# Performance work log

Measured on AMD Instinct MI355X. Metric: run time of the kernel, lower is better.

The kernel has to match this reference:

```python
import jax, jax.numpy as jnp
import numpy as np

B, T, C = 4, 2048, 1024
H = 16
D = C // H  # head_dim = 64
SCALE = D ** -0.5


def setup_inputs() -> dict:
    key = jax.random.key(0)
    k1, k2, k3 = jax.random.split(key, 3)
    x = jax.random.normal(k1, (B, T, C), dtype=jnp.float32)
    w_qkv = jax.random.normal(k2, (C, 3 * C), dtype=jnp.float32) * (C ** -0.5)
    w_proj = jax.random.normal(k3, (C, C), dtype=jnp.float32) * (C ** -0.5)
    return {"x": x, "w_qkv": w_qkv, "w_proj": w_proj}


def reference(x, w_qkv, w_proj):
    Bx, Tx, Cx = x.shape
    qkv = x @ w_qkv                        # [B, T, 3C]
    q, k, v = jnp.split(qkv, 3, axis=-1)   # each [B, T, C]
    # [B, T, H, D] -> [B, H, T, D]
    q = q.reshape(Bx, Tx, H, D).transpose(0, 2, 1, 3)
    k = k.reshape(Bx, Tx, H, D).transpose(0, 2, 1, 3)
    v = v.reshape(Bx, Tx, H, D).transpose(0, 2, 1, 3)
    att = jnp.einsum('bhqd,bhkd->bhqk', q, k) * SCALE  # [B, H, T, T]
    causal = jnp.tril(jnp.ones((Tx, Tx), dtype=bool))
    att = jnp.where(causal[None, None], att, -jnp.inf)
    att = jax.nn.softmax(att, axis=-1)
    # dropout p=0.0 (eval-mode reference): identity
    y = jnp.einsum('bhqk,bhkd->bhqd', att, v)          # [B, H, T, D]
    y = y.transpose(0, 2, 1, 3).reshape(Bx, Tx, Cx)    # [B, T, C]
    return y @ w_proj
```

## Files before the change

### kernel.cpp

```cpp
#include <hip/hip_runtime.h>
#include <hip/hip_bf16.h>

#define Bdim 4
#define Tdim 2048
#define Cdim 1024
#define Hdim 16
#define Ddim 64
#define SCALE_Q 0.18033688011112042f

using f32x4  = __attribute__((ext_vector_type(4))) float;
using short8 = __attribute__((ext_vector_type(8))) short;

union U8 { uint4 v; unsigned short s[8]; };

__device__ __forceinline__ unsigned short f2bf(float f) {
  union { float f; unsigned int i; } x; x.f = f;
  unsigned int lsb = (x.i >> 16) & 1u;
  unsigned int r = x.i + 0x7fffu + lsb;
  return (unsigned short)(r >> 16);
}

__device__ __forceinline__ unsigned int pk_bf16(float lo, float hi) {
  union { __hip_bfloat162 h; unsigned int u; } c;
  c.h = __float22bfloat162_rn(make_float2(lo, hi));
  return c.u;
}

__device__ __forceinline__ float fexp2(float x) {
#if __has_builtin(__builtin_amdgcn_exp2f)
  return __builtin_amdgcn_exp2f(x);
#else
  return exp2f(x);
#endif
}

__device__ __forceinline__ void glds16(const unsigned short* g, unsigned short* l) {
  __builtin_amdgcn_global_load_lds(
      (const __attribute__((address_space(1))) void*)g,
      (__attribute__((address_space(3))) void*)l,
      16, 0, 0);
}

__device__ __forceinline__ int detect_fmt(const unsigned int* xw) {
  int cnt = 0;
  for (int i = 0; i < 64; i++) {
    unsigned int e = (xw[i] >> 7) & 0xFFu;
    if (e >= 100u && e <= 140u) cnt++;
  }
  return (cnt >= 40) ? 1 : 0;
}

__global__ void detect_kernel(const unsigned int* __restrict__ x, int* __restrict__ flag) {
  if (threadIdx.x == 0) *flag = detect_fmt(x);
}

__global__ __launch_bounds__(256) void prep_kernel(
    const void* __restrict__ x, const void* __restrict__ wq, const void* __restrict__ wp,
    unsigned short* __restrict__ X16, unsigned short* __restrict__ WqT,
    unsigned short* __restrict__ WpT, int* __restrict__ flag)
{
  __shared__ __align__(16) unsigned short Ts[64][72];
  __shared__ int sfmt;
  if (threadIdx.x == 0) {
    const int f = detect_fmt((const unsigned int*)x);
    sfmt = f;
    if (blockIdx.x == 0) *flag = f;
  }
  __syncthreads();
  const int fmt = sfmt;
  const unsigned bid = blockIdx.x;
  const int tid = threadIdx.x;

  if (bid < 4096u) {
    const size_t i = (size_t)bid * 256 + tid;
    if (fmt == 1) {
      *(uint4*)(X16 + i * 8) = *(const uint4*)((const unsigned short*)x + i * 8);
    } else {
      const float* s = (const float*)x + i * 8;
      float4 a = *(const float4*)(s);
      float4 b = *(const float4*)(s + 4);
      U8 o;
      o.s[0]=f2bf(a.x); o.s[1]=f2bf(a.y); o.s[2]=f2bf(a.z); o.s[3]=f2bf(a.w);
      o.s[4]=f2bf(b.x); o.s[5]=f2bf(b.y); o.s[6]=f2bf(b.z); o.s[7]=f2bf(b.w);
      *(uint4*)(X16 + i * 8) = o.v;
    }
    return;
  }

  const void* W; unsigned short* WT; int N, K, n0, k0;
  if (bid < 4864u) {
    const int t = bid - 4096;
    W = wq; WT = WqT; N = 3072; K = 1024;
    n0 = (t % 48) * 64; k0 = (t / 48) * 64;
  } else {
    const int t = bid - 4864;
    W = wp; WT = WpT; N = 1024; K = 1024;
    n0 = (t & 15) * 64; k0 = (t >> 4) * 64;
  }
  const int r = tid >> 2, c0 = (tid & 3) * 16;

  if (fmt == 0) {
    const float* Wf = (const float*)W + (size_t)(k0 + r) * N + n0 + c0;
    #pragma unroll
    for (int j4 = 0; j4 < 4; j4++) {
      float4 v = *(const float4*)(Wf + j4 * 4);
      Ts[r][c0 + j4*4 + 0] = f2bf(v.x);
      Ts[r][c0 + j4*4 + 1] = f2bf(v.y);
      Ts[r][c0 + j4*4 + 2] = f2bf(v.z);
      Ts[r][c0 + j4*4 + 3] = f2bf(v.w);
    }
  } else {
    const unsigned short* Wh = (const unsigned short*)W + (size_t)(k0 + r) * N + n0 + c0;
    uint4 v0 = *(const uint4*)(Wh);
    uint4 v1 = *(const uint4*)(Wh + 8);
    *(uint4*)&Ts[r][c0] = v0;
    *(uint4*)&Ts[r][c0 + 8] = v1;
  }
  __syncthreads();

  U8 o0, o1;
  #pragma unroll
  for (int j = 0; j < 8; j++) { o0.s[j] = Ts[c0 + j][r]; o1.s[j] = Ts[c0 + 8 + j][r]; }
  unsigned short* dst = WT + (size_t)(n0 + r) * K + k0 + c0;
  *(uint4*)(dst)     = o0.v;
  *(uint4*)(dst + 8) = o1.v;
}

__global__ __launch_bounds__(256) void gemm128d_kernel(
    const unsigned short* __restrict__ A16,
    const unsigned short* __restrict__ BT16,
    void* __restrict__ Cout,
    unsigned short* __restrict__ Qb,
    unsigned short* __restrict__ Kb,
    unsigned short* __restrict__ Vb,
    const int* __restrict__ flag,
    int M, int N, int K, int mode, int vT)
{
  __shared__ __align__(16) unsigned short As[2][128 * 32];
  __shared__ __align__(16) unsigned short Bs[2][128 * 32];

  const int fmt = *flag;
  const int tid  = threadIdx.x;
  const int wave = tid >> 6;
  const int lane = tid & 63;
  const int col  = lane & 15;
  const int quad = lane >> 4;
  const int m0 = blockIdx.x * 128;
  const int n0 = blockIdx.y * 128;
  const int wm = (wave >> 1) * 64;
  const int wn = (wave & 1) * 64;

  const int r4 = lane >> 2;
  const int schunk = ((lane & 3) ^ ((lane >> 3) & 3)) * 8;
  const int rsw = (quad ^ ((col >> 1) & 3)) * 8;

  f32x4 acc[4][4];
  #pragma unroll
  for (int i = 0; i < 4; i++)
    #pragma unroll
    for (int j = 0; j < 4; j++) acc[i][j] = (f32x4){0.f, 0.f, 0.f, 0.f};

  const unsigned short* ApA = A16  + (size_t)(m0 + wave * 32 + r4) * K + schunk;
  const unsigned short* ApB = ApA + (size_t)16 * K;
  const unsigned short* BpA = BT16 + (size_t)(n0 + wave * 32 + r4) * K + schunk;
  const unsigned short* BpB = BpA + (size_t)16 * K;

#define STAGE(BUF, KS) do { \
    glds16(ApA + (KS) * 32, &As[BUF][wave * 32 * 32]);        \
    glds16(ApB + (KS) * 32, &As[BUF][(wave * 32 + 16) * 32]); \
    glds16(BpA + (KS) * 32, &Bs[BUF][wave * 32 * 32]);        \
    glds16(BpB + (KS) * 32, &Bs[BUF][(wave * 32 + 16) * 32]); \
  } while (0)

#define COMPUTE(BUF) do { \
    short8 afr[4], bfr[4]; \
    _Pragma("unroll") \
    for (int mi = 0; mi < 4; mi++) \
      afr[mi] = *(const short8*)&As[BUF][(wm + mi * 16 + col) * 32 + rsw]; \
    _Pragma("unroll") \
    for (int ni = 0; ni < 4; ni++) \
      bfr[ni] = *(const short8*)&Bs[BUF][(wn + ni * 16 + col) * 32 + rsw]; \
    _Pragma("unroll") \
    for (int mi = 0; mi < 4; mi++) \
      _Pragma("unroll") \
      for (int ni = 0; ni < 4; ni++) \
        acc[mi][ni] = __builtin_amdgcn_mfma_f32_16x16x32_bf16(afr[mi], bfr[ni], acc[mi][ni], 0, 0, 0); \
  } while (0)

  const int NK = K >> 5;
  STAGE(0, 0);
  for (int ks = 0; ks < NK - 1; ++ks) {
    STAGE((ks + 1) & 1, ks + 1);
    asm volatile("s_waitcnt vmcnt(4)" ::: "memory");
    __builtin_amdgcn_s_barrier();
    __builtin_amdgcn_sched_barrier(0);
    COMPUTE(ks & 1);
    __builtin_amdgcn_sched_barrier(0);
    __builtin_amdgcn_s_barrier();
  }
  asm volatile("s_waitcnt vmcnt(0)" ::: "memory");
  __builtin_amdgcn_s_barrier();
  __builtin_amdgcn_sched_barrier(0);
  COMPUTE((NK - 1) & 1);
#undef STAGE
#undef COMPUTE

  if (mode == 1) {
    const int bb = m0 >> 11;
    const int tBase = (m0 & 2047) + wm;
    #pragma unroll
    for (int ni = 0; ni < 4; ni++) {
      const int n = n0 + wn + ni * 16 + col;
      const int which = n >> 10;
      const int rem = n & 1023;
      const int h = rem >> 6;
      const int d = rem & 63;
      if (which == 2 && vT) {
        unsigned short* base = Vb + (size_t)(bb * Hdim + h) * Tdim * Ddim
                                  + (size_t)d * Tdim + tBase;
        #pragma unroll
        for (int mi = 0; mi < 4; mi++) {
          const int t0 = mi * 16 + quad * 4;
          *(uint2*)(base + t0) = make_uint2(pk_bf16(acc[mi][ni][0], acc[mi][ni][1]),
                                            pk_bf16(acc[mi][ni][2], acc[mi][ni][3]));
        }
      } else {
        unsigned short* dstBase = (which == 0) ? Qb : (which == 1 ? Kb : Vb);
        const float scale = (which == 0) ? SCALE_Q : 1.f;
        dstBase += (size_t)(bb * Hdim + h) * Tdim * Ddim + d;
        #pragma unroll
        for (int mi = 0; mi < 4; mi++)
          #pragma unroll
          for (int i = 0; i < 4; i++) {
            const int t = tBase + mi * 16 + quad * 4 + i;
            dstBase[(size_t)t * Ddim] = f2bf(acc[mi][ni][i] * scale);
          }
      }
    }
  } else {
    #pragma unroll
    for (int mi = 0; mi < 4; mi++)
      #pragma unroll
      for (int ni = 0; ni < 4; ni++)
        #pragma unroll
        for (int i = 0; i < 4; i++) {
          const int m = m0 + wm + mi * 16 + quad * 4 + i;
          const int n = n0 + wn + ni * 16 + col;
          const float v = acc[mi][ni][i];
          if (fmt == 0) ((float*)Cout)[(size_t)m * N + n] = v;
          else ((unsigned short*)Cout)[(size_t)m * N + n] = f2bf(v);
        }
  }
}

#define BM 64
#define BN 64
#define BK 32
#define LDK 40

__global__ __launch_bounds__(256) void gemm64_kernel(
    const void* __restrict__ A,
    const void* __restrict__ Bw,
    void* __restrict__ Cout,
    unsigned short* __restrict__ Qb,
    unsigned short* __restrict__ Kb,
    unsigned short* __restrict__ Vb,
    const int* __restrict__ flag,
    int M, int N, int K, int mode, int aFmt, int outFmt, int aOff, int mOff)
{
  __shared__ __align__(16) unsigned short As[BM * LDK];
  __shared__ __align__(16) unsigned short Bs[BN * LDK];

  const int fmt = *flag;
  const int af  = (aFmt  == 2) ? fmt : aFmt;
  const int of  = (outFmt == 2) ? fmt : outFmt;

  const int tid  = threadIdx.x;
  const int wave = tid >> 6;
  const int lane = tid & 63;
  const int m0 = blockIdx.x * BM;
  const int n0 = blockIdx.y * BN;

  const int ar = tid >> 2;
  const int ak = (tid & 3) * 8;
  const int bk = tid >> 3;
  const int bn = (tid & 7) * 8;

  const int lr = lane & 15;
  const int lq = lane >> 4;

  f32x4 acc[4] = {{0,0,0,0},{0,0,0,0},{0,0,0,0},{0,0,0,0}};

  for (int k0 = 0; k0 < K; k0 += BK) {
    U8 a8;
    if (af == 1) {
      a8.v = *(const uint4*)((const unsigned short*)A + (size_t)(aOff + m0 + ar) * K + (k0 + ak));
    } else {
      const float* Af = (const float*)A + (size_t)(aOff + m0 + ar) * K + (k0 + ak);
      float4 x0 = *(const float4*)(Af);
      float4 x1 = *(const float4*)(Af + 4);
      a8.s[0] = f2bf(x0.x); a8.s[1] = f2bf(x0.y); a8.s[2] = f2bf(x0.z); a8.s[3] = f2bf(x0.w);
      a8.s[4] = f2bf(x1.x); a8.s[5] = f2bf(x1.y); a8.s[6] = f2bf(x1.z); a8.s[7] = f2bf(x1.w);
    }
    *(uint4*)(&As[ar * LDK + ak]) = a8.v;

    U8 b8;
    if (fmt == 1) {
      b8.v = *(const uint4*)((const unsigned short*)Bw + (size_t)(k0 + bk) * N + (n0 + bn));
    } else {
      const float* Bf = (const float*)Bw + (size_t)(k0 + bk) * N + (n0 + bn);
      float4 x0 = *(const float4*)(Bf);
      float4 x1 = *(const float4*)(Bf + 4);
      b8.s[0] = f2bf(x0.x); b8.s[1] = f2bf(x0.y); b8.s[2] = f2bf(x0.z); b8.s[3] = f2bf(x0.w);
      b8.s[4] = f2bf(x1.x); b8.s[5] = f2bf(x1.y); b8.s[6] = f2bf(x1.z); b8.s[7] = f2bf(x1.w);
    }
    #pragma unroll
    for (int i = 0; i < 8; i++) Bs[(bn + i) * LDK + bk] = b8.s[i];
    __syncthreads();

    short8 afrag = *(const short8*)(&As[(wave * 16 + lr) * LDK + lq * 8]);
    #pragma unroll
    for (int c = 0; c < 4; c++) {
      short8 bfrag = *(const short8*)(&Bs[(c * 16 + lr) * LDK + lq * 8]);
      acc[c] = __builtin_amdgcn_mfma_f32_16x16x32_bf16(afrag, bfrag, acc[c], 0, 0, 0);
    }
    __syncthreads();
  }

  #pragma unroll
  for (int c = 0; c < 4; c++) {
    #pragma unroll
    for (int i = 0; i < 4; i++) {
      const int m = m0 + wave * 16 + lq * 4 + i;
      const int n = n0 + c * 16 + lr;
      const float v = acc[c][i];
      if (mode == 0) {
        if (of == 0) ((float*)Cout)[(size_t)(mOff + m) * N + n] = v;
        else ((unsigned short*)Cout)[(size_t)(mOff + m) * N + n] = f2bf(v);
      } else {
        const int which = n >> 10;
        const int rem = n & 1023;
        const int h = rem >> 6;
        const int d = rem & 63;
        const int b = m >> 11;
        const int t = m & 2047;
        const size_t idx = ((size_t)(b * Hdim + h) * Tdim + t) * Ddim + d;
        if      (which == 0) Qb[idx] = f2bf(v * SCALE_Q);
        else if (which == 1) Kb[idx] = f2bf(v);
        else                 Vb[idx] = f2bf(v);
      }
    }
  }
}

__global__ __launch_bounds__(256) void attn128_kernel(
    const unsigned short* __restrict__ Qb,
    const unsigned short* __restrict__ Kb,
    const unsigned short* __restrict__ Vb,
    const unsigned short* __restrict__ VbT,
    unsigned short* __restrict__ Y)
{
  __shared__ __align__(16) unsigned short Ks[64 * 72];
  __shared__ __align__(16) unsigned short Vt[64 * 72];
  __shared__ __align__(16) unsigned short Pw[4][32 * 72];

  const int tid  = threadIdx.x;
  const int wave = tid >> 6;
  const int lane = tid & 63;
  const int col  = lane & 15;
  const int quad = lane >> 4;

  const int pair = blockIdx.x & 7;
  const int bh   = blockIdx.x >> 3;
  const size_t headOff = (size_t)bh * Tdim * Ddim;

  const int sr = tid >> 2;
  const int sc = (tid & 3) * 16;

  const int b = bh >> 4;
  const int h = bh & 15;

  const short8 onesf = {16256, 16256, 16256, 16256, 16256, 16256, 16256, 16256};

  #pragma unroll
  for (int half = 0; half < 2; half++) {
    const int qt = half ? (15 - pair) : pair;
    const int qb = qt * 128;
    const int nkt = (qb >> 6) + 2;
    const int rMin = qb + wave * 32;
    const int rMax = rMin + 31;

    short8 qf[2][2];
    #pragma unroll
    for (int mi = 0; mi < 2; mi++) {
      const unsigned short* Qr = Qb + headOff + (size_t)(rMin + mi * 16 + col) * Ddim;
      qf[mi][0] = *(const short8*)(Qr + quad * 8);
      qf[mi][1] = *(const short8*)(Qr + 32 + quad * 8);
    }

    f32x4 o_acc[2][4];
    f32x4 l_acc[2];
    #pragma unroll
    for (int mi = 0; mi < 2; mi++) {
      l_acc[mi] = (f32x4){0.f, 0.f, 0.f, 0.f};
      #pragma unroll
      for (int n = 0; n < 4; n++) o_acc[mi][n] = (f32x4){0.f, 0.f, 0.f, 0.f};
    }

    uint4 kr0, kr1, vr0, vr1;
    {
      const unsigned short* Kr = Kb + headOff + (size_t)sr * Ddim + sc;
      kr0 = *(const uint4*)(Kr);
      kr1 = *(const uint4*)(Kr + 8);
      if (VbT) {
        const unsigned short* Vr = VbT + headOff + (size_t)sr * Tdim + sc;
        vr0 = *(const uint4*)(Vr);
        vr1 = *(const uint4*)(Vr + 8);
      } else {
        const unsigned short* Vr = Vb + headOff + (size_t)sr * Ddim + sc;
        vr0 = *(const uint4*)(Vr);
        vr1 = *(const uint4*)(Vr + 8);
      }
    }

    for (int kt = 0; kt < nkt; kt++) {
      __syncthreads();
      *(uint4*)&Ks[sr * 72 + sc]     = kr0;
      *(uint4*)&Ks[sr * 72 + sc + 8] = kr1;
      if (VbT) {
        *(uint4*)&Vt[sr * 72 + sc]     = vr0;
        *(uint4*)&Vt[sr * 72 + sc + 8] = vr1;
      } else {
        U8 v0, v1; v0.v = vr0; v1.v = vr1;
        #pragma unroll
        for (int j = 0; j < 8; j++) {
          Vt[(sc + j) * 72 + sr]     = v0.s[j];
          Vt[(sc + 8 + j) * 72 + sr] = v1.s[j];
        }
      }
      __syncthreads();

      if (kt + 1 < nkt) {
        const int kb = (kt + 1) * 64;
        const unsigned short* Kr = Kb + headOff + (size_t)(kb + sr) * Ddim + sc;
        kr0 = *(const uint4*)(Kr);
        kr1 = *(const uint4*)(Kr + 8);
        if (VbT) {
          const unsigned short* Vr = VbT + headOff + (size_t)sr * Tdim + kb + sc;
          vr0 = *(const uint4*)(Vr);
          vr1 = *(const uint4*)(Vr + 8);
        } else {
          const unsigned short* Vr = Vb + headOff + (size_t)(kb + sr) * Ddim + sc;
          vr0 = *(const uint4*)(Vr);
          vr1 = *(const uint4*)(Vr + 8);
        }
      }

      const int ktb = kt * 64;
      if (ktb <= rMax) {
        f32x4 s_acc[4][2];
        __builtin_amdgcn_s_setprio(1);
        #pragma unroll
        for (int c = 0; c < 4; c++) {
          const unsigned short* Kl = &Ks[(c * 16 + col) * 72];
          short8 kf0 = *(const short8*)(Kl + quad * 8);
          short8 kf1 = *(const short8*)(Kl + 32 + quad * 8);
          #pragma unroll
          for (int mi = 0; mi < 2; mi++) {
            f32x4 z = {0.f, 0.f, 0.f, 0.f};
            z = __builtin_amdgcn_mfma_f32_16x16x32_bf16(kf0, qf[mi][0], z, 0, 0, 0);
            s_acc[c][mi] = __builtin_amdgcn_mfma_f32_16x16x32_bf16(kf1, qf[mi][1], z, 0, 0, 0);
          }
        }
        __builtin_amdgcn_s_setprio(0);

        if (ktb + 63 > rMin) {
          #pragma unroll
          for (int c = 0; c < 4; c++)
            #pragma unroll
            for (int mi = 0; mi < 2; mi++)
              #pragma unroll
              for (int i = 0; i < 4; i++)
                if (ktb + c * 16 + quad * 4 + i > rMin + mi * 16 + col)
                  s_acc[c][mi][i] = -1e30f;
        }

        #pragma unroll
        for (int mi = 0; mi < 2; mi++)
          #pragma unroll
          for (int c = 0; c < 4; c++) {
            const float p0 = fexp2(fminf(s_acc[c][mi][0], 80.f));
            const float p1 = fexp2(fminf(s_acc[c][mi][1], 80.f));
            const float p2 = fexp2(fminf(s_acc[c][mi][2], 80.f));
            const float p3 = fexp2(fminf(s_acc[c][mi][3], 80.f));
            const unsigned int u0 = pk_bf16(p0, p1);
            const unsigned int u1 = pk_bf16(p2, p3);
            uint2* dst = (uint2*)&Pw[wave][(mi * 16 + col) * 72 + c * 16 + quad * 4];
            *dst = make_uint2(u0, u1);
          }

        short8 pf[2][2];
        __builtin_amdgcn_s_setprio(1);
        #pragma unroll
        for (int mi = 0; mi < 2; mi++) {
          pf[mi][0] = *(const short8*)(&Pw[wave][(mi * 16 + col) * 72 + quad * 8]);
          pf[mi][1] = *(const short8*)(&Pw[wave][(mi * 16 + col) * 72 + 32 + quad * 8]);
          l_acc[mi] = __builtin_amdgcn_mfma_f32_16x16x32_bf16(pf[mi][0], onesf, l_acc[mi], 0, 0, 0);
          l_acc[mi] = __builtin_amdgcn_mfma_f32_16x16x32_bf16(pf[mi][1], onesf, l_acc[mi], 0, 0, 0);
        }
        #pragma unroll
        for (int n = 0; n < 4; n++) {
          const unsigned short* Vl = &Vt[(n * 16 + col) * 72];
          short8 vf0 = *(const short8*)(Vl + quad * 8);
          short8 vf1 = *(const short8*)(Vl + 32 + quad * 8);
          #pragma unroll
          for (int mi = 0; mi < 2; mi++) {
            o_acc[mi][n] = __builtin_amdgcn_mfma_f32_16x16x32_bf16(pf[mi][0], vf0, o_acc[mi][n], 0, 0, 0);
            o_acc[mi][n] = __builtin_amdgcn_mfma_f32_16x16x32_bf16(pf[mi][1], vf1, o_acc[mi][n], 0, 0, 0);
          }
        }
        __builtin_amdgcn_s_setprio(0);
      }
    }

    #pragma unroll
    for (int mi = 0; mi < 2; mi++)
      #pragma unroll
      for (int i = 0; i < 4; i++) {
        const float inv = 1.f / l_acc[mi][i];
        const int qrow = rMin + mi * 16 + quad * 4 + i;
        unsigned short* dst = Y + (size_t)(b * Tdim + qrow) * Cdim + h * Ddim;
        #pragma unroll
        for (int n = 0; n < 4; n++)
          dst[n * 16 + col] = f2bf(o_acc[mi][n][i] * inv);
      }
  }
}

extern "C" void kernel_launch(void* const* d_in, const int* in_sizes, int n_in,
                              void* d_out, int out_size, void* d_ws, size_t ws_size,
                              hipStream_t stream) {
  const void* x      = d_in[0];
  const void* w_qkv  = d_in[1];
  const void* w_proj = d_in[2];

  int* flag = (int*)d_ws;
  unsigned short* wsb = (unsigned short*)((char*)d_ws + 1024);

  const size_t HS = (size_t)Bdim * Hdim * Tdim * Ddim;
  const size_t FULL  = 1024 + 2 * (4 * HS + (size_t)3072 * 1024 + (size_t)1024 * 1024);
  const size_t FULL2 = FULL + 2 * HS;
  const size_t MONO  = 1024 + 2 * (4 * HS);

  dim3 blk(256);

  if (ws_size >= FULL) {
    unsigned short* Qb  = wsb;
    unsigned short* Kb  = Qb + HS;
    unsigned short* Vb  = Kb + HS;
    unsigned short* XY  = Vb + HS;
    unsigned short* WqT = XY + HS;
    unsigned short* WpT = WqT + (size_t)3072 * 1024;
    unsigned short* VbT = WpT + (size_t)1024 * 1024;
    const int M = Bdim * Tdim;

    prep_kernel<<<dim3(5120), blk, 0, stream>>>(x, w_qkv, w_proj, XY, WqT, WpT, flag);

    if (ws_size >= FULL2) {
      gemm128d_kernel<<<dim3(M / 128, 3072 / 128), blk, 0, stream>>>(
          XY, WqT, nullptr, Qb, Kb, VbT, flag, M, 3072, Cdim, 1, 1);
      attn128_kernel<<<dim3(Bdim * Hdim * 8), blk, 0, stream>>>(Qb, Kb, nullptr, VbT, XY);
    } else {
      gemm128d_kernel<<<dim3(M / 128, 3072 / 128), blk, 0, stream>>>(
          XY, WqT, nullptr, Qb, Kb, Vb, flag, M, 3072, Cdim, 1, 0);
      attn128_kernel<<<dim3(Bdim * Hdim * 8), blk, 0, stream>>>(Qb, Kb, Vb, nullptr, XY);
    }

    gemm128d_kernel<<<dim3(M / 128, Cdim / 128), blk, 0, stream>>>(
        XY, WpT, d_out, nullptr, nullptr, nullptr, flag, M, Cdim, Cdim, 0, 0);
  } else if (ws_size >= MONO) {
    detect_kernel<<<1, 64, 0, stream>>>((const unsigned int*)x, flag);
    const size_t HSb = (size_t)Hdim * Tdim * Ddim;
    unsigned short* Qb2 = wsb;
    unsigned short* Kb2 = Qb2 + HSb;
    unsigned short* Vb2 = Kb2 + HSb;
    unsigned short* Y2  = Vb2 + HSb;
    for (int b = 0; b < Bdim; b++) {
      gemm64_kernel<<<dim3(Tdim / BM, 3072 / BN), blk, 0, stream>>>(
          x, w_qkv, nullptr, Qb2, Kb2, Vb2, flag,
          Tdim, 3072, Cdim, 1, 2, 2, b * Tdim, 0);
      attn128_kernel<<<dim3(Hdim * 8), blk, 0, stream>>>(Qb2, Kb2, Vb2, nullptr, Y2);
      gemm64_kernel<<<dim3(Tdim / BM, Cdim / BN), blk, 0, stream>>>(
          Y2, w_proj, d_out, nullptr, nullptr, nullptr, flag,
          Tdim, Cdim, Cdim, 0, 1, 2, 0, b * Tdim);
    }
  } else {
    detect_kernel<<<1, 64, 0, stream>>>((const unsigned int*)x, flag);
    const size_t HSb = (size_t)Hdim * Tdim * Ddim;
    unsigned short* Qb = wsb;
    unsigned short* Kb = Qb + HSb;
    unsigned short* Vb = Kb + HSb;
    unsigned short* Y2 = Vb + HSb;

    for (int b = 0; b < Bdim; b++) {
      gemm64_kernel<<<dim3(Tdim / BM, 3072 / BN), blk, 0, stream>>>(
          x, w_qkv, nullptr, Qb, Kb, Vb, flag,
          Tdim, 3072, Cdim, 1, 2, 2, b * Tdim, 0);

      attn128_kernel<<<dim3(Hdim * 8), blk, 0, stream>>>(Qb, Kb, Vb, nullptr, Y2);

      gemm64_kernel<<<dim3(Tdim / BM, Cdim / BN), blk, 0, stream>>>(
          Y2, w_proj, d_out, nullptr, nullptr, nullptr, flag,
          Tdim, Cdim, Cdim, 0, 1, 2, 0, b * Tdim);
    }
  }
}
```

Before: 249.3 us.

## Double-buffer attention K/V tiles with direct global-to-LDS loads and XOR swizzle

Adds a new attention kernel for the transposed-V path. It double-buffers K and V tiles in LDS, fills them with direct global-to-LDS copies (glds16), and overlaps the next tile's load with the current tile's MFMA work through vmcnt waits. Unpadded LDS rows use an XOR swizzle instead of padding to avoid bank conflicts, and setprio hints are dropped, including from the legacy kernel. The fallback paths keep the old register-staged kernel. LDS use rises from the extra buffer, and there is a barrier at both ends of each tile iteration.

```diff
diff --git a/kernel.cpp b/kernel.cpp
--- a/kernel.cpp
+++ b/kernel.cpp
@@ -356,6 +356,162 @@
 __global__ __launch_bounds__(256) void attn128_kernel(
     const unsigned short* __restrict__ Qb,
     const unsigned short* __restrict__ Kb,
+    const unsigned short* __restrict__ VbT,
+    unsigned short* __restrict__ Y)
+{
+  __shared__ __align__(16) unsigned short Ks[2][64 * 64];
+  __shared__ __align__(16) unsigned short Vt[2][64 * 64];
+  __shared__ __align__(16) unsigned short Pw[4][32 * 64];
+
+  const int tid  = threadIdx.x;
+  const int wave = tid >> 6;
+  const int lane = tid & 63;
+  const int col  = lane & 15;
+  const int quad = lane >> 4;
+  const int cx   = col & 7;
+  const int ch0  = (quad ^ cx) * 8;
+  const int ch1  = ch0 ^ 32;
+
+  const int srow = lane >> 3;
+  const int sx   = ((lane & 7) ^ (srow & 7)) * 8;
+
+  const int pair = blockIdx.x & 7;
+  const int bh   = blockIdx.x >> 3;
+  const size_t headOff = (size_t)bh * Tdim * Ddim;
+  const int b = bh >> 4;
+  const int h = bh & 15;
+
+  const short8 onesf = {16256, 16256, 16256, 16256, 16256, 16256, 16256, 16256};
+
+#define ASTAGE(BUF, KB) do { \
+    const unsigned short* Ksrc = Kb + headOff + (size_t)((KB) + wave * 16 + srow) * Ddim + sx; \
+    glds16(Ksrc,            &Ks[BUF][(wave * 16) * 64]);      \
+    glds16(Ksrc + 8 * Ddim, &Ks[BUF][(wave * 16 + 8) * 64]);  \
+    const unsigned short* Vsrc = VbT + headOff + (size_t)(wave * 16 + srow) * Tdim + (KB) + sx; \
+    glds16(Vsrc,            &Vt[BUF][(wave * 16) * 64]);      \
+    glds16(Vsrc + 8 * Tdim, &Vt[BUF][(wave * 16 + 8) * 64]);  \
+  } while (0)
+
+  #pragma unroll
+  for (int half = 0; half < 2; half++) {
+    const int qt = half ? (15 - pair) : pair;
+    const int qb = qt * 128;
+    const int nkt = (qb >> 6) + 2;
+    const int rMin = qb + wave * 32;
+    const int rMax = rMin + 31;
+
+    short8 qf[2][2];
+    #pragma unroll
+    for (int mi = 0; mi < 2; mi++) {
+      const unsigned short* Qr = Qb + headOff + (size_t)(rMin + mi * 16 + col) * Ddim;
+      qf[mi][0] = *(const short8*)(Qr + quad * 8);
+      qf[mi][1] = *(const short8*)(Qr + 32 + quad * 8);
+    }
+
+    f32x4 o_acc[2][4];
+    f32x4 l_acc[2];
+    #pragma unroll
+    for (int mi = 0; mi < 2; mi++) {
+      l_acc[mi] = (f32x4){0.f, 0.f, 0.f, 0.f};
+      #pragma unroll
+      for (int n = 0; n < 4; n++) o_acc[mi][n] = (f32x4){0.f, 0.f, 0.f, 0.f};
+    }
+
+    ASTAGE(0, 0);
+    for (int kt = 0; kt < nkt; kt++) {
+      const int cur = kt & 1;
+      if (kt + 1 < nkt) {
+        ASTAGE(cur ^ 1, (kt + 1) * 64);
+        asm volatile("s_waitcnt vmcnt(4)" ::: "memory");
+      } else {
+        asm volatile("s_waitcnt vmcnt(0)" ::: "memory");
+      }
+      __builtin_amdgcn_s_barrier();
+      __builtin_amdgcn_sched_barrier(0);
+
+      const int ktb = kt * 64;
+      if (ktb <= rMax) {
+        f32x4 s_acc[4][2];
+        #pragma unroll
+        for (int c = 0; c < 4; c++) {
+          const unsigned short* Kl = &Ks[cur][(c * 16 + col) * 64];
+          short8 kf0 = *(const short8*)(Kl + ch0);
+          short8 kf1 = *(const short8*)(Kl + ch1);
+          #pragma unroll
+          for (int mi = 0; mi < 2; mi++) {
+            f32x4 z = {0.f, 0.f, 0.f, 0.f};
+            z = __builtin_amdgcn_mfma_f32_16x16x32_bf16(kf0, qf[mi][0], z, 0, 0, 0);
+            s_acc[c][mi] = __builtin_amdgcn_mfma_f32_16x16x32_bf16(kf1, qf[mi][1], z, 0, 0, 0);
+          }
+        }
+
+        if (ktb + 63 > rMin) {
+          #pragma unroll
+          for (int c = 0; c < 4; c++)
+            #pragma unroll
+            for (int mi = 0; mi < 2; mi++)
+              #pragma unroll
+              for (int i = 0; i < 4; i++)
+                if (ktb + c * 16 + quad * 4 + i > rMin + mi * 16 + col)
+                  s_acc[c][mi][i] = -1e30f;
+        }
+
+        #pragma unroll
+        for (int mi = 0; mi < 2; mi++)
+          #pragma unroll
+          for (int c = 0; c < 4; c++) {
+            const float p0 = fexp2(fminf(s_acc[c][mi][0], 80.f));
+            const float p1 = fexp2(fminf(s_acc[c][mi][1], 80.f));
+            const float p2 = fexp2(fminf(s_acc[c][mi][2], 80.f));
+            const float p3 = fexp2(fminf(s_acc[c][mi][3], 80.f));
+            const unsigned int u0 = pk_bf16(p0, p1);
+            const unsigned int u1 = pk_bf16(p2, p3);
+            const int po = (((c * 2 + (quad >> 1)) ^ cx) * 8) + (quad & 1) * 4;
+            *(uint2*)&Pw[wave][(mi * 16 + col) * 64 + po] = make_uint2(u0, u1);
+          }
+
+        short8 pf[2][2];
+        #pragma unroll
+        for (int mi = 0; mi < 2; mi++) {
+          pf[mi][0] = *(const short8*)(&Pw[wave][(mi * 16 + col) * 64 + ch0]);
+          pf[mi][1] = *(const short8*)(&Pw[wave][(mi * 16 + col) * 64 + ch1]);
+          l_acc[mi] = __builtin_amdgcn_mfma_f32_16x16x32_bf16(pf[mi][0], onesf, l_acc[mi], 0, 0, 0);
+          l_acc[mi] = __builtin_amdgcn_mfma_f32_16x16x32_bf16(pf[mi][1], onesf, l_acc[mi], 0, 0, 0);
+        }
+        #pragma unroll
+        for (int n = 0; n < 4; n++) {
+          const unsigned short* Vl = &Vt[cur][(n * 16 + col) * 64];
+          short8 vf0 = *(const short8*)(Vl + ch0);
+          short8 vf1 = *(const short8*)(Vl + ch1);
+          #pragma unroll
+          for (int mi = 0; mi < 2; mi++) {
+            o_acc[mi][n] = __builtin_amdgcn_mfma_f32_16x16x32_bf16(pf[mi][0], vf0, o_acc[mi][n], 0, 0, 0);
+            o_acc[mi][n] = __builtin_amdgcn_mfma_f32_16x16x32_bf16(pf[mi][1], vf1, o_acc[mi][n], 0, 0, 0);
+          }
+        }
+      }
+      __builtin_amdgcn_sched_barrier(0);
+      __builtin_amdgcn_s_barrier();
+    }
+
+    #pragma unroll
+    for (int mi = 0; mi < 2; mi++)
+      #pragma unroll
+      for (int i = 0; i < 4; i++) {
+        const float inv = 1.f / l_acc[mi][i];
+        const int qrow = rMin + mi * 16 + quad * 4 + i;
+        unsigned short* dst = Y + (size_t)(b * Tdim + qrow) * Cdim + h * Ddim;
+        #pragma unroll
+        for (int n = 0; n < 4; n++)
+          dst[n * 16 + col] = f2bf(o_acc[mi][n][i] * inv);
+      }
+  }
+#undef ASTAGE
+}
+
+__global__ __launch_bounds__(256) void attn128_legacy_kernel(
+    const unsigned short* __restrict__ Qb,
+    const unsigned short* __restrict__ Kb,
     const unsigned short* __restrict__ Vb,
     const unsigned short* __restrict__ VbT,
     unsigned short* __restrict__ Y)
@@ -459,7 +615,6 @@
       const int ktb = kt * 64;
       if (ktb <= rMax) {
         f32x4 s_acc[4][2];
-        __builtin_amdgcn_s_setprio(1);
         #pragma unroll
         for (int c = 0; c < 4; c++) {
           const unsigned short* Kl = &Ks[(c * 16 + col) * 72];
@@ -472,7 +627,6 @@
             s_acc[c][mi] = __builtin_amdgcn_mfma_f32_16x16x32_bf16(kf1, qf[mi][1], z, 0, 0, 0);
           }
         }
-        __builtin_amdgcn_s_setprio(0);
 
         if (ktb + 63 > rMin) {
           #pragma unroll
@@ -500,7 +654,6 @@
           }
 
         short8 pf[2][2];
-        __builtin_amdgcn_s_setprio(1);
         #pragma unroll
         for (int mi = 0; mi < 2; mi++) {
           pf[mi][0] = *(const short8*)(&Pw[wave][(mi * 16 + col) * 72 + quad * 8]);
@@ -519,7 +672,6 @@
             o_acc[mi][n] = __builtin_amdgcn_mfma_f32_16x16x32_bf16(pf[mi][1], vf1, o_acc[mi][n], 0, 0, 0);
           }
         }
-        __builtin_amdgcn_s_setprio(0);
       }
     }
 
@@ -569,11 +721,11 @@
     if (ws_size >= FULL2) {
       gemm128d_kernel<<<dim3(M / 128, 3072 / 128), blk, 0, stream>>>(
           XY, WqT, nullptr, Qb, Kb, VbT, flag, M, 3072, Cdim, 1, 1);
-      attn128_kernel<<<dim3(Bdim * Hdim * 8), blk, 0, stream>>>(Qb, Kb, nullptr, VbT, XY);
+      attn128_kernel<<<dim3(Bdim * Hdim * 8), blk, 0, stream>>>(Qb, Kb, VbT, XY);
     } else {
       gemm128d_kernel<<<dim3(M / 128, 3072 / 128), blk, 0, stream>>>(
           XY, WqT, nullptr, Qb, Kb, Vb, flag, M, 3072, Cdim, 1, 0);
-      attn128_kernel<<<dim3(Bdim * Hdim * 8), blk, 0, stream>>>(Qb, Kb, Vb, nullptr, XY);
+      attn128_legacy_kernel<<<dim3(Bdim * Hdim * 8), blk, 0, stream>>>(Qb, Kb, Vb, nullptr, XY);
     }
 
     gemm128d_kernel<<<dim3(M / 128, Cdim / 128), blk, 0, stream>>>(
@@ -589,7 +741,7 @@
       gemm64_kernel<<<dim3(Tdim / BM, 3072 / BN), blk, 0, stream>>>(
           x, w_qkv, nullptr, Qb2, Kb2, Vb2, flag,
           Tdim, 3072, Cdim, 1, 2, 2, b * Tdim, 0);
-      attn128_kernel<<<dim3(Hdim * 8), blk, 0, stream>>>(Qb2, Kb2, Vb2, nullptr, Y2);
+      attn128_legacy_kernel<<<dim3(Hdim * 8), blk, 0, stream>>>(Qb2, Kb2, Vb2, nullptr, Y2);
       gemm64_kernel<<<dim3(Tdim / BM, Cdim / BN), blk, 0, stream>>>(
           Y2, w_proj, d_out, nullptr, nullptr, nullptr, flag,
           Tdim, Cdim, Cdim, 0, 1, 2, 0, b * Tdim);
@@ -607,7 +759,7 @@
           x, w_qkv, nullptr, Qb, Kb, Vb, flag,
           Tdim, 3072, Cdim, 1, 2, 2, b * Tdim, 0);
 
-      attn128_kernel<<<dim3(Hdim * 8), blk, 0, stream>>>(Qb, Kb, Vb, nullptr, Y2);
+      attn128_legacy_kernel<<<dim3(Hdim * 8), blk, 0, stream>>>(Qb, Kb, Vb, nullptr, Y2);
 
       gemm64_kernel<<<dim3(Tdim / BM, Cdim / BN), blk, 0, stream>>>(
           Y2, w_proj, d_out, nullptr, nullptr, nullptr, flag,
```

Result: no change. 252.2 us (+1.2%).
